# Kernel optimization log

Measured on AMD Instinct MI355X. Metric: run time of the kernel, lower is better.

## Reference

```python
import jax, jax.numpy as jnp
import numpy as np

EPS = 1e-6

def rms_norm(x, w, eps=EPS):
    # x: [B, L, C]; matches WanRMSNorm: x * rsqrt(mean(x^2) + eps) * weight
    v = jnp.mean(x * x, axis=-1, keepdims=True)
    return x * jax.lax.rsqrt(v + eps) * w

def rope_apply(x, grid_sizes, freqs):
    # x: [B, L, n, d]; freqs: [1024, d//2] angles (original passes e^{i*ang})
    B, L, n, d = x.shape
    c = d // 2
    c1 = c // 3
    c0 = c - 2 * c1
    f0, f1, f2 = freqs[:, :c0], freqs[:, c0:c0 + c1], freqs[:, c0 + c1:]
    gs = np.asarray(grid_sizes)  # concrete per-sample grid sizes (ragged loop)
    outs = []
    for i in range(B):
        f, h, w = int(gs[i, 0]), int(gs[i, 1]), int(gs[i, 2])
        sl = f * h * w
        ang = jnp.concatenate([
            jnp.broadcast_to(f0[:f][:, None, None, :], (f, h, w, c0)),
            jnp.broadcast_to(f1[:h][None, :, None, :], (f, h, w, c1)),
            jnp.broadcast_to(f2[:w][None, None, :, :], (f, h, w, c1)),
        ], axis=-1).reshape(sl, 1, c)
        xi = x[i, :sl].reshape(sl, n, c, 2)  # consecutive pairs = complex (re, im)
        re, im = xi[..., 0], xi[..., 1]
        cs, sn = jnp.cos(ang), jnp.sin(ang)
        rot = jnp.stack([re * cs - im * sn, re * sn + im * cs], axis=-1).reshape(sl, n, d)
        outs.append(jnp.concatenate([rot, x[i, sl:]], axis=0))
    return jnp.stack(outs).astype(jnp.float32)

def attention(q, k, v, seq_lens):
    # full (window_size=(-1,-1)) attention with key-length masking (k_lens)
    B, L, n, d = q.shape
    scale = 1.0 / jnp.sqrt(jnp.asarray(d, jnp.float32))
    scores = jnp.einsum('bqnd,bknd->bnqk', q, k) * scale
    kmask = jnp.arange(L)[None, :] < seq_lens[:, None]  # [B, L]
    scores = jnp.where(kmask[:, None, None, :], scores, jnp.asarray(-1e30, scores.dtype))
    p = jax.nn.softmax(scores, axis=-1)
    return jnp.einsum('bnqk,bknd->bqnd', p, v)


def setup_inputs() -> dict:
    key = jax.random.key(0)
    ks = jax.random.split(key, 8)
    B, L, dim, n = 1, 5000, 1536, 12
    d = dim // n           # 128
    c = d // 2             # 64
    c1 = c // 3            # 21
    c0 = c - 2 * c1        # 22

    x = jax.random.normal(ks[0], (B, L, dim), jnp.float32)
    grid_sizes = jnp.asarray([[8, 25, 25]], jnp.int32)  # F*H*W = 5000 = L
    seq_lens = jnp.full((B,), L, jnp.int32)

    # RoPE angles: pos * base^{-j/size} per (f, h, w) component
    pos = jnp.arange(1024, dtype=jnp.float32)[:, None]
    def comp(sz):
        return pos * (10000.0 ** (-jnp.arange(sz, dtype=jnp.float32) / sz))
    freqs = jnp.concatenate([comp(c0), comp(c1), comp(c1)], axis=1)  # [1024, 64]

    def lin(k):
        return jax.random.normal(k, (dim, dim), jnp.float32) * 0.02
    return {
        'x': x, 'seq_lens': seq_lens, 'grid_sizes': grid_sizes, 'freqs': freqs,
        'Wq': lin(ks[1]), 'bq': jnp.zeros((dim,), jnp.float32),
        'Wk': lin(ks[2]), 'bk': jnp.zeros((dim,), jnp.float32),
        'Wv': lin(ks[3]), 'bv': jnp.zeros((dim,), jnp.float32),
        'Wo': lin(ks[4]), 'bo': jnp.zeros((dim,), jnp.float32),
        'gq': jnp.ones((dim,), jnp.float32),
        'gk': jnp.ones((dim,), jnp.float32),
    }


def reference(x, seq_lens, grid_sizes, freqs, Wq, bq, Wk, bk, Wv, bv, Wo, bo, gq, gk):
    B, L, dim = x.shape
    d = 2 * freqs.shape[1]
    n = dim // d
    q = rms_norm(x @ Wq + bq, gq).reshape(B, L, n, d)
    k = rms_norm(x @ Wk + bk, gk).reshape(B, L, n, d)
    v = (x @ Wv + bv).reshape(B, L, n, d)
    q = rope_apply(q, grid_sizes, freqs)
    k = rope_apply(k, grid_sizes, freqs)
    o = attention(q, k, v, seq_lens)          # [B, L, n, d]
    return o.reshape(B, L, dim) @ Wo + bo
```

## Files before the change

### kernel.cpp

```cpp
#include <hip/hip_runtime.h>

typedef unsigned short u16;
typedef unsigned int   u32;
typedef short bf16x8 __attribute__((ext_vector_type(8)));
typedef float f32x4  __attribute__((ext_vector_type(4)));

__device__ __forceinline__ float b2f(u16 u){ return __uint_as_float(((u32)u) << 16); }
__device__ __forceinline__ u16 f2bf(float f){
  u32 u = __float_as_uint(f);
  return (u16)((u + 0x7fffu + ((u >> 16) & 1u)) >> 16);
}

__device__ __forceinline__ void gload16(const u16* g, u16* l) {
  __builtin_amdgcn_global_load_lds(
      (const __attribute__((address_space(1))) unsigned int*)(g),
      (__attribute__((address_space(3))) unsigned int*)(l), 16, 0, 0);
}

__global__ __launch_bounds__(256) void transpose4(
    const float* __restrict__ Wq, const float* __restrict__ Wk,
    const float* __restrict__ Wv, const float* __restrict__ Wo, u16* __restrict__ wt)
{
  __shared__ float tile[32][33];
  const float* src = blockIdx.z == 0 ? Wq : blockIdx.z == 1 ? Wk : blockIdx.z == 2 ? Wv : Wo;
  u16* dst = wt + (size_t)blockIdx.z * 1536 * 1536;
  const int bx = blockIdx.x * 32, by = blockIdx.y * 32;
  const int tx = threadIdx.x, ty = threadIdx.y;
#pragma unroll
  for (int i = 0; i < 32; i += 8)
    tile[ty + i][tx] = src[(size_t)(by + ty + i) * 1536 + bx + tx];
  __syncthreads();
#pragma unroll
  for (int i = 0; i < 32; i += 8)
    dst[(size_t)(bx + ty + i) * 1536 + by + tx] = f2bf(tile[tx][ty + i]);
}

__global__ __launch_bounds__(256) void cast_f32_bf16(
    const float* __restrict__ src, u16* __restrict__ dst, int n4)
{
  int i = blockIdx.x * 256 + threadIdx.x;
  if (i < n4) {
    float4 f = ((const float4*)src)[i];
    ushort4 o;
    o.x = f2bf(f.x); o.y = f2bf(f.y); o.z = f2bf(f.z); o.w = f2bf(f.w);
    ((ushort4*)dst)[i] = o;
  }
}

__global__ __launch_bounds__(256) void transpose_v(
    const u16* __restrict__ src, u16* __restrict__ dst, int L, int Lpad)
{
  __shared__ u16 tile[64][72];
  const int kb = blockIdx.x * 64, c0 = blockIdx.y * 64;
  const int tid = threadIdx.x;
#pragma unroll
  for (int i = 0; i < 2; i++) {
    int slot = tid + i * 256;
    int row = slot >> 3, oct = slot & 7;
    bf16x8 z = {0, 0, 0, 0, 0, 0, 0, 0};
    int key = kb + row;
    if (key < L) z = *(const bf16x8*)(src + (size_t)key * 1536 + c0 + oct * 8);
    *(bf16x8*)&tile[row][oct * 8] = z;
  }
  __syncthreads();
#pragma unroll
  for (int i = 0; i < 2; i++) {
    int slot = tid + i * 256;
    int d = slot >> 3, oct = slot & 7;
    bf16x8 z;
#pragma unroll
    for (int j = 0; j < 8; j++) z[j] = (short)tile[oct * 8 + j][d];
    *(bf16x8*)(dst + (size_t)(c0 + d) * Lpad + kb + oct * 8) = z;
  }
}

template<bool F32OUT>
__device__ __forceinline__ void gemm_core(
    const u16* __restrict__ A, const u16* __restrict__ BT,
    const float* __restrict__ bias, void* __restrict__ Cv, int M,
    int m0, int n0)
{
  __shared__ u16 As[2][128][32];
  __shared__ u16 Bs[2][128][32];
  const int tid = threadIdx.x;
  const int wave = tid >> 6, lane = tid & 63;
  const int wm = (wave & 1) * 64, wn = (wave >> 1) * 64;
  const int l16 = lane & 15, quad = lane >> 4;

  const int srow = lane >> 2, scol = (lane & 3) * 8;
  const u16* ap0 = A  + (size_t)(m0 + wave * 32 + srow) * 1536 + scol;
  const u16* ap1 = ap0 + (size_t)16 * 1536;
  const u16* bp0 = BT + (size_t)(n0 + wave * 32 + srow) * 1536 + scol;
  const u16* bp1 = bp0 + (size_t)16 * 1536;

#define STAGE_GEMM(curb) do { \
    gload16(ap0, &As[curb][wave * 32][0]); \
    gload16(ap1, &As[curb][wave * 32 + 16][0]); \
    gload16(bp0, &Bs[curb][wave * 32][0]); \
    gload16(bp1, &Bs[curb][wave * 32 + 16][0]); \
    ap0 += 32; ap1 += 32; bp0 += 32; bp1 += 32; } while (0)

  f32x4 acc[4][4] = {};
  STAGE_GEMM(0);
  for (int ks = 0; ks < 48; ks++) {
    const int cur = ks & 1;
    if (ks + 1 < 48) {
      STAGE_GEMM(cur ^ 1);
      asm volatile("s_waitcnt vmcnt(4)" ::: "memory");
    } else {
      asm volatile("s_waitcnt vmcnt(0)" ::: "memory");
    }
    __builtin_amdgcn_s_barrier();
    __builtin_amdgcn_sched_barrier(0);
    bf16x8 af[4], bfr[4];
#pragma unroll
    for (int mt = 0; mt < 4; mt++) af[mt] = *(const bf16x8*)&As[cur][wm + mt * 16 + l16][quad * 8];
#pragma unroll
    for (int nt = 0; nt < 4; nt++) bfr[nt] = *(const bf16x8*)&Bs[cur][wn + nt * 16 + l16][quad * 8];
#pragma unroll
    for (int mt = 0; mt < 4; mt++)
#pragma unroll
      for (int nt = 0; nt < 4; nt++)
        acc[mt][nt] = __builtin_amdgcn_mfma_f32_16x16x32_bf16(af[mt], bfr[nt], acc[mt][nt], 0, 0, 0);
    __builtin_amdgcn_s_barrier();
  }
#undef STAGE_GEMM

#pragma unroll
  for (int nt = 0; nt < 4; nt++) {
    int col = n0 + wn + nt * 16 + l16;
    float bv = bias[col];
#pragma unroll
    for (int mt = 0; mt < 4; mt++) {
      int rowb = m0 + wm + mt * 16 + quad * 4;
#pragma unroll
      for (int r = 0; r < 4; r++) {
        int row = rowb + r;
        if (row < M) {
          float val = acc[mt][nt][r] + bv;
          if (F32OUT) ((float*)Cv)[(size_t)row * 1536 + col] = val;
          else        ((u16*)Cv)[(size_t)row * 1536 + col] = f2bf(val);
        }
      }
    }
  }
}

__global__ __launch_bounds__(256) void gemm_qkv(
    const u16* __restrict__ A, const u16* __restrict__ wt,
    const float* __restrict__ bq, const float* __restrict__ bk, const float* __restrict__ bv,
    u16* __restrict__ outbase, int M, size_t SZW, size_t SZT)
{
  const int z = blockIdx.z;
  const u16* BT = wt + (size_t)z * SZW;
  const float* bias = z == 0 ? bq : z == 1 ? bk : bv;
  u16* C = outbase + (size_t)z * SZT;
  gemm_core<false>(A, BT, bias, C, M, blockIdx.x * 128, blockIdx.y * 128);
}

__global__ __launch_bounds__(256) void gemm_out(
    const u16* __restrict__ A, const u16* __restrict__ BT,
    const float* __restrict__ bias, float* __restrict__ C, int M)
{
  gemm_core<true>(A, BT, bias, C, M, blockIdx.x * 128, blockIdx.y * 128);
}

__global__ __launch_bounds__(256) void rmsrope(
    u16* __restrict__ qb, u16* __restrict__ kb,
    const float* __restrict__ gq, const float* __restrict__ gk,
    const float* __restrict__ freqs, const int* __restrict__ gsz)
{
  const int s = blockIdx.x, tid = threadIdx.x;
  const size_t base = (size_t)s * 1536;
  float qv[6], kv[6];
  float sq = 0.f, sk = 0.f;
#pragma unroll
  for (int i = 0; i < 6; i++) {
    float a = b2f(qb[base + tid * 6 + i]); qv[i] = a; sq += a * a;
    float b = b2f(kb[base + tid * 6 + i]); kv[i] = b; sk += b * b;
  }
#pragma unroll
  for (int d2 = 1; d2 < 64; d2 <<= 1) { sq += __shfl_xor(sq, d2); sk += __shfl_xor(sk, d2); }
  __shared__ float red[8];
  const int wave = tid >> 6, lane = tid & 63;
  if (lane == 0) { red[wave] = sq; red[4 + wave] = sk; }
  __syncthreads();
  sq = red[0] + red[1] + red[2] + red[3];
  sk = red[4] + red[5] + red[6] + red[7];
  const float rq = rsqrtf(sq * (1.f / 1536.f) + 1e-6f);
  const float rk = rsqrtf(sk * (1.f / 1536.f) + 1e-6f);
  const int F = gsz[0], H = gsz[1], W = gsz[2];
  const int sl = F * H * W;
  const bool rope = s < sl;
  int pf = 0, ph = 0, pw = 0;
  if (rope) { pf = s / (H * W); int rr = s - pf * (H * W); ph = rr / W; pw = rr - ph * W; }
#pragma unroll
  for (int pp = 0; pp < 3; pp++) {
    const int j0 = tid * 6 + pp * 2;
    float qre = qv[pp * 2]     * rq * gq[j0];
    float qim = qv[pp * 2 + 1] * rq * gq[j0 + 1];
    float kre = kv[pp * 2]     * rk * gk[j0];
    float kim = kv[pp * 2 + 1] * rk * gk[j0 + 1];
    if (rope) {
      const int ti = (j0 & 127) >> 1;
      const int pos = ti < 22 ? pf : (ti < 43 ? ph : pw);
      const float ang = freqs[pos * 64 + ti];
      const float cs = cosf(ang), sn = sinf(ang);
      float t1 = qre * cs - qim * sn; qim = qre * sn + qim * cs; qre = t1;
      float t2 = kre * cs - kim * sn; kim = kre * sn + kim * cs; kre = t2;
    }
    qb[base + j0] = f2bf(qre); qb[base + j0 + 1] = f2bf(qim);
    kb[base + j0] = f2bf(kre); kb[base + j0 + 1] = f2bf(kim);
  }
}

__global__ __launch_bounds__(256, 2) void attn_mfma(
    const u16* __restrict__ q, const u16* __restrict__ k, const u16* __restrict__ vt,
    u16* __restrict__ o, const int* __restrict__ seq_lens, int L, int Lpad)
{
  __shared__ u16 Ks[64][136];
  __shared__ u16 Vs[128][72];
  __shared__ u16 Pl[4][32][72];
  const int tid = threadIdx.x, wave = tid >> 6, lane = tid & 63;
  const int l16 = lane & 15, quad = lane >> 4;
  const int h = blockIdx.y;
  const int seqlen = seq_lens[0];
  const int q0 = blockIdx.x * 128 + wave * 32;
  const float SC = 0.12752551286084934f;

  int krow[4], kcol[4], vd[4], voct[4];
#pragma unroll
  for (int i = 0; i < 4; i++) {
    int slot = tid + i * 256;
    krow[i] = slot >> 4; kcol[i] = (slot & 15) * 8;
    vd[i]   = slot >> 3; voct[i] = (slot & 7) * 8;
  }
  const u16* kp  = k + h * 128;
  const u16* vtp = vt + (size_t)h * 128 * Lpad;

  bf16x8 Qf[2][4];
#pragma unroll
  for (int qg = 0; qg < 2; qg++) {
    int qr = q0 + qg * 16 + l16;
#pragma unroll
    for (int ds = 0; ds < 4; ds++) {
      bf16x8 z = {0, 0, 0, 0, 0, 0, 0, 0};
      if (qr < L) {
        bf16x8 raw = *(const bf16x8*)(q + (size_t)qr * 1536 + h * 128 + ds * 32 + quad * 8);
#pragma unroll
        for (int j = 0; j < 8; j++) z[j] = (short)f2bf(b2f((u16)raw[j]) * SC);
      }
      Qf[qg][ds] = z;
    }
  }
  f32x4 accO[2][8] = {};
  float m_i[2] = {-1e30f, -1e30f}, l_i[2] = {0.f, 0.f};

  const int ntile = (seqlen + 63) >> 6;
  bf16x8 kpre[4], vpre[4];
#pragma unroll
  for (int i = 0; i < 4; i++) {
    int row = krow[i];
    bf16x8 z = {0, 0, 0, 0, 0, 0, 0, 0};
    if (row < seqlen) z = *(const bf16x8*)(kp + (size_t)row * 1536 + kcol[i]);
    kpre[i] = z;
    vpre[i] = *(const bf16x8*)(vtp + (size_t)vd[i] * Lpad + voct[i]);
  }

  for (int t = 0; t < ntile; t++) {
    const int kb = t * 64;
    __syncthreads();
#pragma unroll
    for (int i = 0; i < 4; i++) {
      *(bf16x8*)&Ks[krow[i]][kcol[i]] = kpre[i];
      *(bf16x8*)&Vs[vd[i]][voct[i]]   = vpre[i];
    }
    __syncthreads();
    if (t + 1 < ntile) {
      const int kb2 = kb + 64;
#pragma unroll
      for (int i = 0; i < 4; i++) {
        int row = kb2 + krow[i];
        bf16x8 z = {0, 0, 0, 0, 0, 0, 0, 0};
        if (row < seqlen) z = *(const bf16x8*)(kp + (size_t)row * 1536 + kcol[i]);
        kpre[i] = z;
        vpre[i] = *(const bf16x8*)(vtp + (size_t)vd[i] * Lpad + kb2 + voct[i]);
      }
    }

    const bool full = (kb + 64 <= seqlen);
    float sv[2][16];
    float tmax[2] = {-1e30f, -1e30f};
#pragma unroll
    for (int kt = 0; kt < 4; kt++) {
      f32x4 a0 = {0.f, 0.f, 0.f, 0.f};
      f32x4 a1 = {0.f, 0.f, 0.f, 0.f};
#pragma unroll
      for (int ds = 0; ds < 4; ds++) {
        bf16x8 kf = *(const bf16x8*)&Ks[kt * 16 + l16][ds * 32 + quad * 8];
        a0 = __builtin_amdgcn_mfma_f32_16x16x32_bf16(kf, Qf[0][ds], a0, 0, 0, 0);
        a1 = __builtin_amdgcn_mfma_f32_16x16x32_bf16(kf, Qf[1][ds], a1, 0, 0, 0);
      }
      if (full) {
#pragma unroll
        for (int r = 0; r < 4; r++) {
          sv[0][kt * 4 + r] = a0[r]; tmax[0] = fmaxf(tmax[0], a0[r]);
          sv[1][kt * 4 + r] = a1[r]; tmax[1] = fmaxf(tmax[1], a1[r]);
        }
      } else {
#pragma unroll
        for (int r = 0; r < 4; r++) {
          int key = kb + kt * 16 + quad * 4 + r;
          float s0 = (key < seqlen) ? a0[r] : -1e30f;
          float s1 = (key < seqlen) ? a1[r] : -1e30f;
          sv[0][kt * 4 + r] = s0; tmax[0] = fmaxf(tmax[0], s0);
          sv[1][kt * 4 + r] = s1; tmax[1] = fmaxf(tmax[1], s1);
        }
      }
    }
    float alpha[2] = {1.f, 1.f};
    bool resc[2];
#pragma unroll
    for (int qg = 0; qg < 2; qg++) {
      float tm = tmax[qg];
      tm = fmaxf(tm, __shfl_xor(tm, 16));
      tm = fmaxf(tm, __shfl_xor(tm, 32));
      resc[qg] = !__all(tm - m_i[qg] <= 8.f);
      float mnew = m_i[qg];
      if (resc[qg]) {
        mnew = fmaxf(m_i[qg], tm);
        alpha[qg] = exp2f(m_i[qg] - mnew);
      }
      float psum = 0.f;
      u16 pk[16];
#pragma unroll
      for (int i2 = 0; i2 < 16; i2++) {
        float p = exp2f(sv[qg][i2] - mnew);
        u32 pu = __float_as_uint(p) & 0xffff0000u;
        psum += __uint_as_float(pu);
        pk[i2] = (u16)(pu >> 16);
      }
      psum += __shfl_xor(psum, 16);
      psum += __shfl_xor(psum, 32);
      l_i[qg] = (resc[qg] ? l_i[qg] * alpha[qg] : l_i[qg]) + psum;
      m_i[qg] = mnew;
#pragma unroll
      for (int kt = 0; kt < 4; kt++) {
        ushort4 w4 = { pk[kt * 4], pk[kt * 4 + 1], pk[kt * 4 + 2], pk[kt * 4 + 3] };
        *(ushort4*)&Pl[wave][qg * 16 + l16][kt * 16 + quad * 4] = w4;
      }
    }
#pragma unroll
    for (int qg = 0; qg < 2; qg++) {
      if (resc[qg]) {
        float ar[4];
#pragma unroll
        for (int r = 0; r < 4; r++) ar[r] = __shfl(alpha[qg], quad * 4 + r);
#pragma unroll
        for (int dt = 0; dt < 8; dt++)
#pragma unroll
          for (int r = 0; r < 4; r++) accO[qg][dt][r] *= ar[r];
      }
    }
    bf16x8 pf00 = *(const bf16x8*)&Pl[wave][l16][quad * 8];
    bf16x8 pf01 = *(const bf16x8*)&Pl[wave][l16][32 + quad * 8];
    bf16x8 pf10 = *(const bf16x8*)&Pl[wave][16 + l16][quad * 8];
    bf16x8 pf11 = *(const bf16x8*)&Pl[wave][16 + l16][32 + quad * 8];
#pragma unroll
    for (int dt = 0; dt < 8; dt++) {
      bf16x8 vf0 = *(const bf16x8*)&Vs[dt * 16 + l16][quad * 8];
      bf16x8 vf1 = *(const bf16x8*)&Vs[dt * 16 + l16][32 + quad * 8];
      accO[0][dt] = __builtin_amdgcn_mfma_f32_16x16x32_bf16(pf00, vf0, accO[0][dt], 0, 0, 0);
      accO[0][dt] = __builtin_amdgcn_mfma_f32_16x16x32_bf16(pf01, vf1, accO[0][dt], 0, 0, 0);
      accO[1][dt] = __builtin_amdgcn_mfma_f32_16x16x32_bf16(pf10, vf0, accO[1][dt], 0, 0, 0);
      accO[1][dt] = __builtin_amdgcn_mfma_f32_16x16x32_bf16(pf11, vf1, accO[1][dt], 0, 0, 0);
    }
  }
#pragma unroll
  for (int qg = 0; qg < 2; qg++) {
    float linv[4];
#pragma unroll
    for (int r = 0; r < 4; r++) linv[r] = 1.f / __shfl(l_i[qg], quad * 4 + r);
#pragma unroll
    for (int r = 0; r < 4; r++) {
      int qr = q0 + qg * 16 + quad * 4 + r;
      if (qr < L) {
#pragma unroll
        for (int dt = 0; dt < 8; dt++)
          o[(size_t)qr * 1536 + h * 128 + dt * 16 + l16] = f2bf(accO[qg][dt][r] * linv[r]);
      }
    }
  }
}

extern "C" void kernel_launch(void* const* d_in, const int* in_sizes, int n_in,
                              void* d_out, int out_size, void* d_ws, size_t ws_size,
                              hipStream_t stream) {
  const float* x      = (const float*)d_in[0];
  const int* seq_lens = (const int*)d_in[1];
  const int* gsz      = (const int*)d_in[2];
  const float* freqs  = (const float*)d_in[3];
  const float* Wq     = (const float*)d_in[4];
  const float* bq     = (const float*)d_in[5];
  const float* Wk     = (const float*)d_in[6];
  const float* bk     = (const float*)d_in[7];
  const float* Wv     = (const float*)d_in[8];
  const float* bv     = (const float*)d_in[9];
  const float* Wo     = (const float*)d_in[10];
  const float* bo     = (const float*)d_in[11];
  const float* gq     = (const float*)d_in[12];
  const float* gk     = (const float*)d_in[13];
  float* out = (float*)d_out;

  const int DIM = 1536;
  const int L = in_sizes[0] / DIM;
  const int Lpad = ((L + 63) / 64) * 64;
  const size_t SZW = (size_t)DIM * DIM;
  const size_t SZT = (size_t)L * DIM;

  u16* wt   = (u16*)d_ws;
  u16* xb   = wt + 4 * SZW;
  u16* attn = xb + SZT;
  u16* qraw = attn + SZT;
  u16* kraw = qraw + SZT;
  u16* vraw = kraw + SZT;
  u16* vtb  = vraw + SZT;

  const int mtiles = (L + 127) / 128;

  transpose4<<<dim3(48, 48, 4), dim3(32, 8), 0, stream>>>(Wq, Wk, Wv, Wo, wt);
  cast_f32_bf16<<<(int)((SZT / 4 + 255) / 256), 256, 0, stream>>>(x, xb, (int)(SZT / 4));
  gemm_qkv<<<dim3(mtiles, 12, 3), 256, 0, stream>>>(xb, wt, bq, bk, bv, qraw, L, SZW, SZT);
  rmsrope<<<dim3(L), 256, 0, stream>>>(qraw, kraw, gq, gk, freqs, gsz);
  transpose_v<<<dim3((L + 63) / 64, DIM / 64), 256, 0, stream>>>(vraw, vtb, L, Lpad);
  attn_mfma<<<dim3((L + 127) / 128, 12), 256, 0, stream>>>(qraw, kraw, vtb, attn, seq_lens, L, Lpad);
  gemm_out<<<dim3(mtiles, 12), 256, 0, stream>>>(attn, wt + 3 * SZW, bo, out, L);
}
```

Before: 557.7 us.

## Split attention over two key halves with combine kernel and swizzled K LDS

New measurement: 1.087 ms. 1.95x slower.

```diff
diff --git a/kernel.cpp b/kernel.cpp
--- a/kernel.cpp
+++ b/kernel.cpp
@@ -214,27 +214,31 @@
   }
 }
 
-__global__ __launch_bounds__(256, 2) void attn_mfma(
+__global__ __launch_bounds__(256, 3) void attn_mfma(
     const u16* __restrict__ q, const u16* __restrict__ k, const u16* __restrict__ vt,
-    u16* __restrict__ o, const int* __restrict__ seq_lens, int L, int Lpad)
-{
-  __shared__ u16 Ks[64][136];
+    u16* __restrict__ o0, u16* __restrict__ o1, float* __restrict__ ml,
+    const int* __restrict__ seq_lens, int L, int Lpad)
+{
+  __shared__ u16 Ks[64][128];
   __shared__ u16 Vs[128][72];
   __shared__ u16 Pl[4][32][72];
   const int tid = threadIdx.x, wave = tid >> 6, lane = tid & 63;
   const int l16 = lane & 15, quad = lane >> 4;
   const int h = blockIdx.y;
+  const int sp = blockIdx.z;
   const int seqlen = seq_lens[0];
   const int q0 = blockIdx.x * 128 + wave * 32;
   const float SC = 0.12752551286084934f;
 
-  int krow[4], kcol[4], vd[4], voct[4];
+  int krow[4], kcolg[4], kcolx[4], vd[4], voct[4];
 #pragma unroll
   for (int i = 0; i < 4; i++) {
     int slot = tid + i * 256;
-    krow[i] = slot >> 4; kcol[i] = (slot & 15) * 8;
+    krow[i] = slot >> 4; kcolg[i] = (slot & 15) * 8;
+    kcolx[i] = kcolg[i] ^ ((krow[i] & 7) << 3);
     vd[i]   = slot >> 3; voct[i] = (slot & 7) * 8;
   }
+  const int ksw = (l16 & 7) << 3;
   const u16* kp  = k + h * 128;
   const u16* vtp = vt + (size_t)h * 128 * Lpad;
 
@@ -257,32 +261,39 @@
   float m_i[2] = {-1e30f, -1e30f}, l_i[2] = {0.f, 0.f};
 
   const int ntile = (seqlen + 63) >> 6;
+  const int th = (ntile + 1) >> 1;
+  const int t0 = sp * th;
+  const int t1 = (ntile < t0 + th) ? ntile : (t0 + th);
+
   bf16x8 kpre[4], vpre[4];
-#pragma unroll
-  for (int i = 0; i < 4; i++) {
-    int row = krow[i];
-    bf16x8 z = {0, 0, 0, 0, 0, 0, 0, 0};
-    if (row < seqlen) z = *(const bf16x8*)(kp + (size_t)row * 1536 + kcol[i]);
-    kpre[i] = z;
-    vpre[i] = *(const bf16x8*)(vtp + (size_t)vd[i] * Lpad + voct[i]);
-  }
-
-  for (int t = 0; t < ntile; t++) {
+  if (t0 < t1) {
+    const int kb0 = t0 * 64;
+#pragma unroll
+    for (int i = 0; i < 4; i++) {
+      int row = kb0 + krow[i];
+      bf16x8 z = {0, 0, 0, 0, 0, 0, 0, 0};
+      if (row < seqlen) z = *(const bf16x8*)(kp + (size_t)row * 1536 + kcolg[i]);
+      kpre[i] = z;
+      vpre[i] = *(const bf16x8*)(vtp + (size_t)vd[i] * Lpad + kb0 + voct[i]);
+    }
+  }
+
+  for (int t = t0; t < t1; t++) {
     const int kb = t * 64;
     __syncthreads();
 #pragma unroll
     for (int i = 0; i < 4; i++) {
-      *(bf16x8*)&Ks[krow[i]][kcol[i]] = kpre[i];
+      *(bf16x8*)&Ks[krow[i]][kcolx[i]] = kpre[i];
       *(bf16x8*)&Vs[vd[i]][voct[i]]   = vpre[i];
     }
     __syncthreads();
-    if (t + 1 < ntile) {
+    if (t + 1 < t1) {
       const int kb2 = kb + 64;
 #pragma unroll
       for (int i = 0; i < 4; i++) {
         int row = kb2 + krow[i];
         bf16x8 z = {0, 0, 0, 0, 0, 0, 0, 0};
-        if (row < seqlen) z = *(const bf16x8*)(kp + (size_t)row * 1536 + kcol[i]);
+        if (row < seqlen) z = *(const bf16x8*)(kp + (size_t)row * 1536 + kcolg[i]);
         kpre[i] = z;
         vpre[i] = *(const bf16x8*)(vtp + (size_t)vd[i] * Lpad + kb2 + voct[i]);
       }
@@ -297,7 +308,7 @@
       f32x4 a1 = {0.f, 0.f, 0.f, 0.f};
 #pragma unroll
       for (int ds = 0; ds < 4; ds++) {
-        bf16x8 kf = *(const bf16x8*)&Ks[kt * 16 + l16][ds * 32 + quad * 8];
+        bf16x8 kf = *(const bf16x8*)&Ks[kt * 16 + l16][(ds * 32 + quad * 8) ^ ksw];
         a0 = __builtin_amdgcn_mfma_f32_16x16x32_bf16(kf, Qf[0][ds], a0, 0, 0, 0);
         a1 = __builtin_amdgcn_mfma_f32_16x16x32_bf16(kf, Qf[1][ds], a1, 0, 0, 0);
       }
@@ -376,21 +387,61 @@
       accO[1][dt] = __builtin_amdgcn_mfma_f32_16x16x32_bf16(pf11, vf1, accO[1][dt], 0, 0, 0);
     }
   }
+  u16* op = sp == 0 ? o0 : o1;
+  float* mlp = ml + (size_t)sp * L * 24;
 #pragma unroll
   for (int qg = 0; qg < 2; qg++) {
+    if (quad == 0) {
+      int qr = q0 + qg * 16 + l16;
+      if (qr < L) {
+        size_t mi = ((size_t)qr * 12 + h) * 2;
+        mlp[mi] = m_i[qg]; mlp[mi + 1] = l_i[qg];
+      }
+    }
     float linv[4];
 #pragma unroll
-    for (int r = 0; r < 4; r++) linv[r] = 1.f / __shfl(l_i[qg], quad * 4 + r);
+    for (int r = 0; r < 4; r++) {
+      float lv = __shfl(l_i[qg], quad * 4 + r);
+      linv[r] = lv > 0.f ? 1.f / lv : 0.f;
+    }
 #pragma unroll
     for (int r = 0; r < 4; r++) {
       int qr = q0 + qg * 16 + quad * 4 + r;
       if (qr < L) {
 #pragma unroll
         for (int dt = 0; dt < 8; dt++)
-          o[(size_t)qr * 1536 + h * 128 + dt * 16 + l16] = f2bf(accO[qg][dt][r] * linv[r]);
-      }
-    }
-  }
+          op[(size_t)qr * 1536 + h * 128 + dt * 16 + l16] = f2bf(accO[qg][dt][r] * linv[r]);
+      }
+    }
+  }
+}
+
+__global__ __launch_bounds__(256) void attn_combine(
+    u16* __restrict__ o0, const u16* __restrict__ o1,
+    const float* __restrict__ ml, int L)
+{
+  int idx = blockIdx.x * 256 + threadIdx.x;
+  int total = L * 192;
+  if (idx >= total) return;
+  int q = idx / 192, g = idx - q * 192;
+  int h = g >> 4;
+  size_t mi = ((size_t)q * 12 + h) * 2;
+  size_t ms = (size_t)L * 24;
+  float m0 = ml[mi], l0 = ml[mi + 1];
+  float m1 = ml[ms + mi], l1 = ml[ms + mi + 1];
+  float m = fmaxf(m0, m1);
+  float w0 = l0 > 0.f ? l0 * exp2f(m0 - m) : 0.f;
+  float w1 = l1 > 0.f ? l1 * exp2f(m1 - m) : 0.f;
+  float inv = 1.f / (w0 + w1);
+  w0 *= inv; w1 *= inv;
+  size_t off = (size_t)idx * 8;
+  bf16x8 a = *(const bf16x8*)(o0 + off);
+  bf16x8 b = *(const bf16x8*)(o1 + off);
+  bf16x8 r;
+#pragma unroll
+  for (int j = 0; j < 8; j++)
+    r[j] = (short)f2bf(w0 * b2f((u16)a[j]) + w1 * b2f((u16)b[j]));
+  *(bf16x8*)(o0 + off) = r;
 }
 
 extern "C" void kernel_launch(void* const* d_in, const int* in_sizes, int n_in,
@@ -425,6 +476,7 @@
   u16* kraw = qraw + SZT;
   u16* vraw = kraw + SZT;
   u16* vtb  = vraw + SZT;
+  float* ml = (float*)vraw;
 
   const int mtiles = (L + 127) / 128;
 
@@ -433,6 +485,8 @@
   gemm_qkv<<<dim3(mtiles, 12, 3), 256, 0, stream>>>(xb, wt, bq, bk, bv, qraw, L, SZW, SZT);
   rmsrope<<<dim3(L), 256, 0, stream>>>(qraw, kraw, gq, gk, freqs, gsz);
   transpose_v<<<dim3((L + 63) / 64, DIM / 64), 256, 0, stream>>>(vraw, vtb, L, Lpad);
-  attn_mfma<<<dim3((L + 127) / 128, 12), 256, 0, stream>>>(qraw, kraw, vtb, attn, seq_lens, L, Lpad);
+  attn_mfma<<<dim3((L + 127) / 128, 12, 2), 256, 0, stream>>>(
+      qraw, kraw, vtb, attn, xb, ml, seq_lens, L, Lpad);
+  attn_combine<<<(L * 192 + 255) / 256, 256, 0, stream>>>(attn, xb, ml, L);
   gemm_out<<<dim3(mtiles, 12), 256, 0, stream>>>(attn, wt + 3 * SZW, bo, out, L);
 }
```
